# Kernel tuning notes

Hardware: AMD Instinct MI355X
Metric: run time of the kernel (lower is better)

## Reference

```python
import jax, jax.numpy as jnp
import numpy as np

HIDDEN = 1024
B, S = 4, 2048


def setup_inputs() -> dict:
    key = jax.random.key(0)
    ks = jax.random.split(key, 9)
    scale = 1.0 / np.sqrt(HIDDEN)
    mk = lambda k: (jax.random.normal(k, (HIDDEN, HIDDEN), dtype=jnp.float32) * scale)
    return {
        "x": jax.random.normal(ks[0], (B, S, HIDDEN), dtype=jnp.float32),
        "Wq": mk(ks[1]), "bq": jnp.zeros((HIDDEN,), jnp.float32),
        "Wk": mk(ks[2]), "bk": jnp.zeros((HIDDEN,), jnp.float32),
        "Wv": mk(ks[3]), "bv": jnp.zeros((HIDDEN,), jnp.float32),
        "Wo": mk(ks[4]), "bo": jnp.zeros((HIDDEN,), jnp.float32),
    }


def reference(x, Wq, bq, Wk, bk, Wv, bv, Wo, bo):
    # Single-head attention over the full hidden dim (num_heads unused in source).
    # Linear(H,H): y = x @ W^T + b ; weights stored [out,in] torch-style.
    q = jnp.einsum("bsh,oh->bso", x, Wq) + bq  # [B,S,H]
    k = jnp.einsum("bsh,oh->bso", x, Wk) + bk
    v = jnp.einsum("bsh,oh->bso", x, Wv) + bv
    scores = jnp.einsum("bqh,bkh->bqk", q, k) / jnp.sqrt(jnp.float32(HIDDEN))
    attn = jax.nn.softmax(scores, axis=-1)  # dropout rate is 0.0 (eval-equivalent)
    ctx = jnp.einsum("bqk,bkh->bqh", attn, v)
    return jnp.einsum("bsh,oh->bso", ctx, Wo) + bo
```

## Files before the change

### kernel.cpp

```cpp
#include <hip/hip_runtime.h>

#define HID 1024
#define SEQ 2048
#define NB 4
#define BS 8192

typedef __attribute__((ext_vector_type(8))) short short8;
typedef __attribute__((ext_vector_type(8))) unsigned short ushort8;
typedef __attribute__((ext_vector_type(4))) float f32x4;

__device__ __forceinline__ float bf2f(unsigned short u) {
  unsigned int x = ((unsigned int)u) << 16;
  return __builtin_bit_cast(float, x);
}
__device__ __forceinline__ unsigned short f2bf(float f) {
  unsigned int x = __builtin_bit_cast(unsigned int, f);
  x = x + 0x7fffu + ((x >> 16) & 1u);
  return (unsigned short)(x >> 16);
}

#define GLOAD16(g, l)                                                          \
  __builtin_amdgcn_global_load_lds(                                            \
      (const __attribute__((address_space(1))) unsigned int*)(g),              \
      (__attribute__((address_space(3))) unsigned int*)(l), 16, 0, 0)

__global__ void cast_f32_to_bf16(const float* __restrict__ in,
                                 unsigned short* __restrict__ out, int n) {
  int i = (blockIdx.x * 256 + threadIdx.x) * 8;
  if (i >= n) return;
  f32x4 a = *(const f32x4*)(in + i);
  f32x4 b = *(const f32x4*)(in + i + 4);
  ushort8 o;
  o[0] = f2bf(a[0]); o[1] = f2bf(a[1]); o[2] = f2bf(a[2]); o[3] = f2bf(a[3]);
  o[4] = f2bf(b[0]); o[5] = f2bf(b[1]); o[6] = f2bf(b[2]); o[7] = f2bf(b[3]);
  *(ushort8*)(out + i) = o;
}

template <int BN, int OUT_F32, int BIAS_MODE>
__global__ __launch_bounds__(512, 2) void gemm8p(
    const unsigned short* __restrict__ A, const unsigned short* __restrict__ B,
    void* __restrict__ Cv, const float* __restrict__ bias,
    const float* __restrict__ bias2, int K, int lda, int ldb, int ldc,
    long long bsA, long long bsB, long long bsC, float alpha) {
  static_assert(BN == 256 || BN == 128, "BN");
  constexpr int WMW = (BN == 256) ? 2 : 4;
  constexpr int WNW = 8 / WMW;
  constexpr int MF = 8 / WMW;
  constexpr int NF = 2;
  constexpr int NBH = BN / 2;
  constexpr int GB = (BN == 256) ? 2 : 1;
  constexpr int VMS = 2 + GB;
  constexpr int BSLOT = NBH * 64;

  __shared__ unsigned short ldsA[4 * 8192];
  __shared__ unsigned short ldsB[4 * BSLOT];

  const int tid = threadIdx.x;
  const int lane = tid & 63, wid = tid >> 6;
  const int fr = lane & 15, fq = lane >> 4;
  const int wm = wid / WNW, wn = wid % WNW;
  const int bx = blockIdx.x, by = blockIdx.y, bz = blockIdx.z;
  const unsigned short* Ag = A + bz * bsA + (long long)by * 256 * lda;
  const unsigned short* Bg = B + bz * bsB + (long long)bx * BN * ldb;
  const int NT = K >> 6;

  const int La0 = wid * 1024 + lane * 16;
  const int La1 = 8192 + La0;
  const int Pa0 = La0 ^ ((La0 >> 4) & 0x70);
  const int Pa1 = La1 ^ ((La1 >> 4) & 0x70);
  const int aR0 = Pa0 >> 7, aC0 = (Pa0 & 127) >> 1;
  const int aR1 = Pa1 >> 7, aC1 = (Pa1 & 127) >> 1;

  auto stageA = [&](int tile, int h) {
    if (tile >= NT) return;
    unsigned short* d = &ldsA[(((tile & 1) << 1) | h) * 8192 + wid * 512];
    GLOAD16(Ag + (long long)(h * 128 + aR0) * lda + tile * 64 + aC0, d);
    GLOAD16(Ag + (long long)(h * 128 + aR1) * lda + tile * 64 + aC1, d + 4096);
  };
  auto stageB = [&](int tile, int h) {
    if (tile >= NT) return;
    unsigned short* d = &ldsB[(((tile & 1) << 1) | h) * BSLOT + wid * 512];
    GLOAD16(Bg + (long long)(h * NBH + aR0) * ldb + tile * 64 + aC0, d);
    if (GB == 2)
      GLOAD16(Bg + (long long)(h * NBH + aR1) * ldb + tile * 64 + aC1, d + 4096);
  };

  int offA[MF][2], offB[NF][2];
#pragma unroll
  for (int i = 0; i < MF; ++i)
#pragma unroll
    for (int s = 0; s < 2; ++s) {
      int b = (wm * (128 / WMW) + i * 16 + fr) * 128 + s * 64 + fq * 16;
      offA[i][s] = (b ^ ((b >> 4) & 0x70)) >> 1;
    }
#pragma unroll
  for (int n = 0; n < NF; ++n)
#pragma unroll
    for (int s = 0; s < 2; ++s) {
      int b = (wn * 32 + n * 16 + fr) * 128 + s * 64 + fq * 16;
      offB[n][s] = (b ^ ((b >> 4) & 0x70)) >> 1;
    }

  f32x4 acc[2][2][MF][NF] = {};

  stageA(0, 0); stageB(0, 0); stageA(0, 1); stageB(0, 1);
  stageA(1, 0); stageB(1, 0);
  asm volatile("s_waitcnt vmcnt(%0)" ::"i"(VMS) : "memory");
  __builtin_amdgcn_s_barrier();

  for (int kt = 0; kt < NT; kt += 2) {
#pragma unroll
    for (int t2 = 0; t2 < 2; ++t2) {
      const int buf = (kt + t2) & 1;
#pragma unroll
      for (int ph = 0; ph < 4; ++ph) {
        const int mh = ph >> 1, nh = ph & 1;
        const int p = t2 * 4 + ph;
        short8 av[MF][2], bw[NF][2];
        const unsigned short* pa = &ldsA[((buf << 1) | mh) * 8192];
        const unsigned short* pb = &ldsB[((buf << 1) | nh) * BSLOT];
#pragma unroll
        for (int i = 0; i < MF; ++i)
#pragma unroll
          for (int s = 0; s < 2; ++s)
            av[i][s] = *(const short8*)(pa + offA[i][s]);
#pragma unroll
        for (int n = 0; n < NF; ++n)
#pragma unroll
          for (int s = 0; s < 2; ++s)
            bw[n][s] = *(const short8*)(pb + offB[n][s]);
        if (p == 0) stageA(kt + 1, 1);
        else if (p == 1) stageB(kt + 1, 1);
        else if (p == 2) stageA(kt + 2, 0);
        else if (p == 3) stageB(kt + 2, 0);
        else if (p == 4) stageA(kt + 2, 1);
        else if (p == 5) stageB(kt + 2, 1);
        else if (p == 6) stageA(kt + 3, 0);
        else stageB(kt + 3, 0);
        __builtin_amdgcn_s_barrier();
        __builtin_amdgcn_s_setprio(1);
#pragma unroll
        for (int i = 0; i < MF; ++i)
#pragma unroll
          for (int n = 0; n < NF; ++n)
#pragma unroll
            for (int s = 0; s < 2; ++s)
              acc[mh][nh][i][n] = __builtin_amdgcn_mfma_f32_16x16x32_bf16(
                  av[i][s], bw[n][s], acc[mh][nh][i][n], 0, 0, 0);
        __builtin_amdgcn_s_setprio(0);
        if (p == 3) {
          if (kt + 2 < NT)
            asm volatile("s_waitcnt vmcnt(%0)" ::"i"(VMS) : "memory");
          else
            asm volatile("s_waitcnt vmcnt(0)" ::: "memory");
        }
        if (p == 7) {
          if (kt + 3 < NT)
            asm volatile("s_waitcnt vmcnt(%0)" ::"i"(VMS) : "memory");
          else
            asm volatile("s_waitcnt vmcnt(0)" ::: "memory");
        }
        __builtin_amdgcn_s_barrier();
      }
    }
  }

  const long long cb0 = (long long)bz * bsC;
#pragma unroll
  for (int mh = 0; mh < 2; ++mh)
#pragma unroll
    for (int nh = 0; nh < 2; ++nh)
#pragma unroll
      for (int i = 0; i < MF; ++i)
#pragma unroll
        for (int n = 0; n < NF; ++n) {
          const int col = bx * BN + nh * NBH + wn * 32 + n * 16 + fr;
          float cbias = 0.f;
          if (BIAS_MODE == 1) cbias = bias[col];
          if (BIAS_MODE == 3)
            cbias = (col < 1024) ? bias[col] : bias2[col - 1024];
#pragma unroll
          for (int j = 0; j < 4; ++j) {
            const int row =
                by * 256 + mh * 128 + wm * (128 / WMW) + i * 16 + fq * 4 + j;
            float v = acc[mh][nh][i][n][j] * alpha + cbias;
            if (BIAS_MODE == 2) v += bias[row];
            const long long idx = cb0 + (long long)row * ldc + col;
            if (OUT_F32)
              ((float*)Cv)[idx] = v;
            else
              ((unsigned short*)Cv)[idx] = f2bf(v);
          }
        }
}

__global__ __launch_bounds__(256) void softmax_inplace(
    unsigned short* __restrict__ P) {
  __shared__ float red[8];
  unsigned short* p = P + (long long)blockIdx.x * 2048;
  const int tid = threadIdx.x;
  const int lane = tid & 63, w = tid >> 6;
  ushort8 v = *(const ushort8*)(p + tid * 8);
  float f[8];
#pragma unroll
  for (int i = 0; i < 8; ++i) f[i] = bf2f(v[i]);
  float mx = f[0];
#pragma unroll
  for (int i = 1; i < 8; ++i) mx = fmaxf(mx, f[i]);
#pragma unroll
  for (int off = 32; off >= 1; off >>= 1)
    mx = fmaxf(mx, __shfl_xor(mx, off, 64));
  if (lane == 0) red[w] = mx;
  __syncthreads();
  mx = fmaxf(fmaxf(red[0], red[1]), fmaxf(red[2], red[3]));
  float s = 0.f;
#pragma unroll
  for (int i = 0; i < 8; ++i) {
    f[i] = __expf(f[i] - mx);
    s += f[i];
  }
#pragma unroll
  for (int off = 32; off >= 1; off >>= 1) s += __shfl_xor(s, off, 64);
  if (lane == 0) red[4 + w] = s;
  __syncthreads();
  s = (red[4] + red[5]) + (red[6] + red[7]);
  const float inv = 1.0f / s;
  ushort8 o;
#pragma unroll
  for (int i = 0; i < 8; ++i) o[i] = f2bf(f[i] * inv);
  *(ushort8*)(p + tid * 8) = o;
}

extern "C" void kernel_launch(void* const* d_in, const int* in_sizes, int n_in,
                              void* d_out, int out_size, void* d_ws,
                              size_t ws_size, hipStream_t stream) {
  (void)in_sizes; (void)n_in; (void)out_size; (void)ws_size;
  const float* x = (const float*)d_in[0];
  const float* Wq = (const float*)d_in[1];
  const float* bq = (const float*)d_in[2];
  const float* Wk = (const float*)d_in[3];
  const float* bk = (const float*)d_in[4];
  const float* Wv = (const float*)d_in[5];
  const float* bv = (const float*)d_in[6];
  const float* Wo = (const float*)d_in[7];
  const float* bo = (const float*)d_in[8];
  float* out = (float*)d_out;

  char* ws = (char*)d_ws;
  unsigned short* xbf  = (unsigned short*)(ws + 0);
  unsigned short* wqk  = (unsigned short*)(ws + 16777216);
  unsigned short* wvbf = (unsigned short*)(ws + 20971520);
  unsigned short* wobf = (unsigned short*)(ws + 23068672);
  unsigned short* QKb  = (unsigned short*)(ws + 25165824);
  unsigned short* Vt   = (unsigned short*)(ws + 58720256);
  unsigned short* ctxb = (unsigned short*)(ws + 75497472);
  unsigned short* P    = (unsigned short*)(ws + 92274688);

  cast_f32_to_bf16<<<4096, 256, 0, stream>>>(x, xbf, BS * HID);
  cast_f32_to_bf16<<<512, 256, 0, stream>>>(Wq, wqk, HID * HID);
  cast_f32_to_bf16<<<512, 256, 0, stream>>>(Wk, wqk + HID * HID, HID * HID);
  cast_f32_to_bf16<<<512, 256, 0, stream>>>(Wv, wvbf, HID * HID);
  cast_f32_to_bf16<<<512, 256, 0, stream>>>(Wo, wobf, HID * HID);

  gemm8p<256, 0, 3><<<dim3(8, 32, 1), 512, 0, stream>>>(
      xbf, wqk, QKb, bq, bk, HID, HID, HID, 2048, 0, 0, 0, 1.0f);
  gemm8p<128, 0, 2><<<dim3(64, 4, 1), 512, 0, stream>>>(
      wvbf, xbf, Vt, bv, nullptr, HID, HID, HID, BS, 0, 0, 0, 1.0f);
  gemm8p<256, 0, 0><<<dim3(8, 8, NB), 512, 0, stream>>>(
      QKb, QKb + 1024, P, nullptr, nullptr, HID, 2048, 2048, SEQ,
      (long long)SEQ * 2048, (long long)SEQ * 2048, (long long)SEQ * SEQ,
      0.03125f);
  softmax_inplace<<<BS, 256, 0, stream>>>(P);
  gemm8p<128, 0, 0><<<dim3(8, 8, NB), 512, 0, stream>>>(
      P, Vt, ctxb, nullptr, nullptr, SEQ, SEQ, BS, HID,
      (long long)SEQ * SEQ, (long long)SEQ, (long long)SEQ * HID, 1.0f);
  gemm8p<128, 1, 1><<<dim3(8, 32, 1), 512, 0, stream>>>(
      ctxb, wobf, out, bo, nullptr, HID, HID, HID, HID, 0, 0, 0, 1.0f);
}
```

Baseline: 240.0 us.

## Fold Wo into V projection, remap workgroups, and relax vmcnt waits

Computes Wo·Wv once as a combined weight so V' = x·(WoWv)^T, then P·V' directly yields the output with a fused bias Wo·bv+bo. This removes the separate ctx→output GEMM (8192x1024x1024) and replaces it with a small 1024^3 weight product. It also adds an XCD-aware workgroup index remap and finer-grained s_waitcnt placement in the GEMM pipeline. The weight product is rounded to bf16, which changes numerics slightly.

```diff
diff --git a/kernel.cpp b/kernel.cpp
--- a/kernel.cpp
+++ b/kernel.cpp
@@ -23,6 +23,11 @@
   __builtin_amdgcn_global_load_lds(                                            \
       (const __attribute__((address_space(1))) unsigned int*)(g),              \
       (__attribute__((address_space(3))) unsigned int*)(l), 16, 0, 0)
+
+template <int N>
+__device__ __forceinline__ void vmwait() {
+  asm volatile("s_waitcnt vmcnt(%0)" ::"i"(N) : "memory");
+}
 
 __global__ void cast_f32_to_bf16(const float* __restrict__ in,
                                  unsigned short* __restrict__ out, int n) {
@@ -34,6 +39,30 @@
   o[0] = f2bf(a[0]); o[1] = f2bf(a[1]); o[2] = f2bf(a[2]); o[3] = f2bf(a[3]);
   o[4] = f2bf(b[0]); o[5] = f2bf(b[1]); o[6] = f2bf(b[2]); o[7] = f2bf(b[3]);
   *(ushort8*)(out + i) = o;
+}
+
+__global__ __launch_bounds__(256) void transpose_cast(
+    const float* __restrict__ in, unsigned short* __restrict__ out) {
+  __shared__ float t[32][33];
+  const int bx = blockIdx.x * 32, by = blockIdx.y * 32;
+  const int tx = threadIdx.x & 31, ty = threadIdx.x >> 5;
+#pragma unroll
+  for (int i = 0; i < 4; ++i)
+    t[ty + i * 8][tx] = in[(by + ty + i * 8) * 1024 + bx + tx];
+  __syncthreads();
+#pragma unroll
+  for (int i = 0; i < 4; ++i)
+    out[(bx + ty + i * 8) * 1024 + by + tx] = f2bf(t[tx][ty + i * 8]);
+}
+
+__global__ __launch_bounds__(256) void bias_fuse(const float* __restrict__ Wo,
+                                                 const float* __restrict__ bv,
+                                                 const float* __restrict__ bo,
+                                                 float* __restrict__ bp) {
+  const int h = blockIdx.x * 256 + threadIdx.x;
+  float s = bo[h];
+  for (int k = 0; k < 1024; ++k) s += Wo[h * 1024 + k] * bv[k];
+  bp[h] = s;
 }
 
 template <int BN, int OUT_F32, int BIAS_MODE>
@@ -49,8 +78,10 @@
   constexpr int NF = 2;
   constexpr int NBH = BN / 2;
   constexpr int GB = (BN == 256) ? 2 : 1;
-  constexpr int VMS = 2 + GB;
   constexpr int BSLOT = NBH * 64;
+  constexpr int WK0 = (BN == 256) ? 6 : 5;
+  constexpr int WK3 = (BN == 256) ? 8 : 6;
+  constexpr int WPR = (BN == 256) ? 4 : 3;
 
   __shared__ unsigned short ldsA[4 * 8192];
   __shared__ unsigned short ldsB[4 * BSLOT];
@@ -59,7 +90,14 @@
   const int lane = tid & 63, wid = tid >> 6;
   const int fr = lane & 15, fq = lane >> 4;
   const int wm = wid / WNW, wn = wid % WNW;
-  const int bx = blockIdx.x, by = blockIdx.y, bz = blockIdx.z;
+
+  const int nx = gridDim.x;
+  const int nwg = nx * gridDim.y;
+  int f = blockIdx.y * nx + blockIdx.x;
+  f = (f & 7) * (nwg >> 3) + (f >> 3);
+  const int bx = f % nx, by = f / nx;
+  const int bz = blockIdx.z;
+
   const unsigned short* Ag = A + bz * bsA + (long long)by * 256 * lda;
   const unsigned short* Bg = B + bz * bsB + (long long)bx * BN * ldb;
   const int NT = K >> 6;
@@ -105,10 +143,11 @@
 
   stageA(0, 0); stageB(0, 0); stageA(0, 1); stageB(0, 1);
   stageA(1, 0); stageB(1, 0);
-  asm volatile("s_waitcnt vmcnt(%0)" ::"i"(VMS) : "memory");
+  vmwait<WPR>();
   __builtin_amdgcn_s_barrier();
 
   for (int kt = 0; kt < NT; kt += 2) {
+    const bool tail = (kt + 2 >= NT);
 #pragma unroll
     for (int t2 = 0; t2 < 2; ++t2) {
       const int buf = (kt + t2) & 1;
@@ -148,18 +187,10 @@
               acc[mh][nh][i][n] = __builtin_amdgcn_mfma_f32_16x16x32_bf16(
                   av[i][s], bw[n][s], acc[mh][nh][i][n], 0, 0, 0);
         __builtin_amdgcn_s_setprio(0);
-        if (p == 3) {
-          if (kt + 2 < NT)
-            asm volatile("s_waitcnt vmcnt(%0)" ::"i"(VMS) : "memory");
-          else
-            asm volatile("s_waitcnt vmcnt(0)" ::: "memory");
-        }
-        if (p == 7) {
-          if (kt + 3 < NT)
-            asm volatile("s_waitcnt vmcnt(%0)" ::"i"(VMS) : "memory");
-          else
-            asm volatile("s_waitcnt vmcnt(0)" ::: "memory");
-        }
+        if (p == 0) vmwait<WK0>();
+        else if (p == 3) { if (tail) vmwait<0>(); else vmwait<WK3>(); }
+        else if (p == 4) { if (tail) vmwait<0>(); else vmwait<WK0>(); }
+        else if (p == 7) vmwait<WK3>();
         __builtin_amdgcn_s_barrier();
       }
     }
@@ -249,31 +280,33 @@
   char* ws = (char*)d_ws;
   unsigned short* xbf  = (unsigned short*)(ws + 0);
   unsigned short* wqk  = (unsigned short*)(ws + 16777216);
-  unsigned short* wvbf = (unsigned short*)(ws + 20971520);
-  unsigned short* wobf = (unsigned short*)(ws + 23068672);
-  unsigned short* QKb  = (unsigned short*)(ws + 25165824);
-  unsigned short* Vt   = (unsigned short*)(ws + 58720256);
-  unsigned short* ctxb = (unsigned short*)(ws + 75497472);
-  unsigned short* P    = (unsigned short*)(ws + 92274688);
+  unsigned short* wobf = (unsigned short*)(ws + 20971520);
+  unsigned short* wvT  = (unsigned short*)(ws + 23068672);
+  unsigned short* wov  = (unsigned short*)(ws + 25165824);
+  float*          bpr  = (float*)        (ws + 27262976);
+  unsigned short* VWoT = (unsigned short*)(ws + 33554432);
+  unsigned short* QKb  = (unsigned short*)(ws + 50331648);
+  unsigned short* P    = (unsigned short*)(ws + 83886080);
 
   cast_f32_to_bf16<<<4096, 256, 0, stream>>>(x, xbf, BS * HID);
   cast_f32_to_bf16<<<512, 256, 0, stream>>>(Wq, wqk, HID * HID);
   cast_f32_to_bf16<<<512, 256, 0, stream>>>(Wk, wqk + HID * HID, HID * HID);
-  cast_f32_to_bf16<<<512, 256, 0, stream>>>(Wv, wvbf, HID * HID);
   cast_f32_to_bf16<<<512, 256, 0, stream>>>(Wo, wobf, HID * HID);
-
+  transpose_cast<<<dim3(32, 32), 256, 0, stream>>>(Wv, wvT);
+  bias_fuse<<<4, 256, 0, stream>>>(Wo, bv, bo, bpr);
+
+  gemm8p<128, 0, 0><<<dim3(8, 4, 1), 512, 0, stream>>>(
+      wobf, wvT, wov, nullptr, nullptr, HID, HID, HID, HID, 0, 0, 0, 1.0f);
+  gemm8p<128, 0, 0><<<dim3(64, 4, 1), 512, 0, stream>>>(
+      wov, xbf, VWoT, nullptr, nullptr, HID, HID, HID, BS, 0, 0, 0, 1.0f);
   gemm8p<256, 0, 3><<<dim3(8, 32, 1), 512, 0, stream>>>(
       xbf, wqk, QKb, bq, bk, HID, HID, HID, 2048, 0, 0, 0, 1.0f);
-  gemm8p<128, 0, 2><<<dim3(64, 4, 1), 512, 0, stream>>>(
-      wvbf, xbf, Vt, bv, nullptr, HID, HID, HID, BS, 0, 0, 0, 1.0f);
   gemm8p<256, 0, 0><<<dim3(8, 8, NB), 512, 0, stream>>>(
       QKb, QKb + 1024, P, nullptr, nullptr, HID, 2048, 2048, SEQ,
       (long long)SEQ * 2048, (long long)SEQ * 2048, (long long)SEQ * SEQ,
       0.03125f);
   softmax_inplace<<<BS, 256, 0, stream>>>(P);
-  gemm8p<128, 0, 0><<<dim3(8, 8, NB), 512, 0, stream>>>(
-      P, Vt, ctxb, nullptr, nullptr, SEQ, SEQ, BS, HID,
-      (long long)SEQ * SEQ, (long long)SEQ, (long long)SEQ * HID, 1.0f);
-  gemm8p<128, 1, 1><<<dim3(8, 32, 1), 512, 0, stream>>>(
-      ctxb, wobf, out, bo, nullptr, HID, HID, HID, HID, 0, 0, 0, 1.0f);
-}
+  gemm8p<128, 1, 1><<<dim3(8, 8, NB), 512, 0, stream>>>(
+      P, VWoT, out, bpr, nullptr, SEQ, SEQ, BS, HID, (long long)SEQ * SEQ,
+      (long long)SEQ, (long long)SEQ * HID, 1.0f);
+}
```

Measured after the change: 255.8 us. 1.07x slower.
